# Optimization experiments

Hardware: AMD Instinct MI355X
Metric: run time of the kernel (lower is better)

## Reference

```python
import jax, jax.numpy as jnp
import numpy as np

N = 16384          # tokens
D = 2048           # model dim
SQRT_K = 64        # per-factor codebook size
K = SQRT_K * SQRT_K  # num_experts = 4096
TOP_K = 8
GATE_RANK = 16


def setup_inputs() -> dict:
    key = jax.random.key(0)
    k_x, k_w1, k_w2, k_wg, k_g = jax.random.split(key, 5)
    x = jax.random.normal(k_x, (N, D), dtype=jnp.float32)
    # nn.Linear(d, sqrt_K, bias=False) weights: [out, in]
    W1 = jax.random.normal(k_w1, (SQRT_K, D), dtype=jnp.float32) * (1.0 / np.sqrt(D))
    W2 = jax.random.normal(k_w2, (SQRT_K, D), dtype=jnp.float32) * (1.0 / np.sqrt(D))
    Wg = jax.random.normal(k_wg, (GATE_RANK, D), dtype=jnp.float32) * (1.0 / np.sqrt(D))
    # gate_keys: Parameter(randn(K, gate_rank) * 0.01)
    G = jax.random.normal(k_g, (K, GATE_RANK), dtype=jnp.float32) * 0.01
    return {"x": x, "W1": W1, "W2": W2, "Wg": Wg, "G": G}


def reference(x, W1, W2, Wg, G):
    # Stage 1: product-key selection scores
    s1 = x @ W1.T                                   # [N, sqrt_K]
    s2 = x @ W2.T                                   # [N, sqrt_K]
    select_scores = (s1[:, :, None] + s2[:, None, :]).reshape(x.shape[0], -1)  # [N, K]
    select_topk_vals, topk_idx = jax.lax.top_k(select_scores, TOP_K)           # [N, top_k]

    # Stage 2: low-rank gate calibration
    q_g = x @ Wg.T                                  # [N, r_g]
    gate_full = q_g @ G.T                           # [N, K]
    gate_topk = jnp.take_along_axis(gate_full, topk_idx, axis=-1)              # [N, top_k]

    combined = select_topk_vals + gate_topk
    topk_weights = jax.nn.softmax(combined, axis=-1)
    return topk_idx, topk_weights, select_scores
```

## Files before the change

### kernel.cpp

```cpp
#include <hip/hip_runtime.h>
#include <math.h>
#include <float.h>

#define NTOK  16384
#define DDIM  2048
#define TOPK  8
#define GR    16

#define MB    32
#define KB    64
#define WS_ST 148
#define XS_ST 34
#define S_ST  148
#define LDSF  (KB*WS_ST + KB*XS_ST)

__device__ __forceinline__ void insert8(float v[TOPK], int id[TOPK], float nv, int nk)
{
    bool beats_last = (nv > v[TOPK-1]) || (nv == v[TOPK-1] && nk < id[TOPK-1]);
    if (!beats_last) return;
    v[TOPK-1] = nv; id[TOPK-1] = nk;
    #pragma unroll
    for (int q = TOPK-1; q > 0; --q) {
        bool sw = (v[q] > v[q-1]) || (v[q] == v[q-1] && id[q] < id[q-1]);
        if (sw) {
            float tv = v[q]; v[q] = v[q-1]; v[q-1] = tv;
            int   ti = id[q]; id[q] = id[q-1]; id[q-1] = ti;
        }
    }
}

__global__ __launch_bounds__(256, 2) void pk_router(
    const float* __restrict__ x,  const float* __restrict__ W1,
    const float* __restrict__ W2, const float* __restrict__ Wg,
    const float* __restrict__ G,  float* __restrict__ out)
{
    __shared__ float lds[LDSF];
    const int t    = threadIdx.x;
    const int rb   = blockIdx.x * MB;
    const int rowg = t & 15;
    const int colg = t >> 4;

    float acc1[2][4];
    float acc2[2][4];
    float accg[2];
    #pragma unroll
    for (int r = 0; r < 2; ++r) {
        #pragma unroll
        for (int u = 0; u < 4; ++u) { acc1[r][u] = 0.f; acc2[r][u] = 0.f; }
        accg[r] = 0.f;
    }

    float* xs = lds + KB*WS_ST;

    for (int kb = 0; kb < DDIM; kb += KB) {
        #pragma unroll
        for (int i = 0; i < 2; ++i) {
            const int idx = t + 256*i;
            const int r   = idx >> 4;
            const int k4  = idx & 15;
            const float4 v = *(const float4*)(x + (size_t)(rb + r)*DDIM + kb + k4*4);
            xs[(k4*4+0)*XS_ST + r] = v.x;
            xs[(k4*4+1)*XS_ST + r] = v.y;
            xs[(k4*4+2)*XS_ST + r] = v.z;
            xs[(k4*4+3)*XS_ST + r] = v.w;
        }
        #pragma unroll
        for (int i = 0; i < 9; ++i) {
            const int idx = t + 256*i;
            const int c   = idx >> 4;
            const int k4  = idx & 15;
            const float* src = (c < 64)  ? (W1 + (size_t)c*DDIM)
                             : (c < 128) ? (W2 + (size_t)(c-64)*DDIM)
                                         : (Wg + (size_t)(c-128)*DDIM);
            const float4 v = *(const float4*)(src + kb + k4*4);
            lds[(k4*4+0)*WS_ST + c] = v.x;
            lds[(k4*4+1)*WS_ST + c] = v.y;
            lds[(k4*4+2)*WS_ST + c] = v.z;
            lds[(k4*4+3)*WS_ST + c] = v.w;
        }
        __syncthreads();

        #pragma unroll 8
        for (int kk = 0; kk < KB; ++kk) {
            const float2 a  = *(const float2*)(xs + kk*XS_ST + rowg*2);
            const float4 b1 = *(const float4*)(lds + kk*WS_ST + colg*4);
            const float4 b2 = *(const float4*)(lds + kk*WS_ST + 64 + colg*4);
            const float  bg = lds[kk*WS_ST + 128 + colg];
            acc1[0][0] += a.x*b1.x; acc1[0][1] += a.x*b1.y;
            acc1[0][2] += a.x*b1.z; acc1[0][3] += a.x*b1.w;
            acc1[1][0] += a.y*b1.x; acc1[1][1] += a.y*b1.y;
            acc1[1][2] += a.y*b1.z; acc1[1][3] += a.y*b1.w;
            acc2[0][0] += a.x*b2.x; acc2[0][1] += a.x*b2.y;
            acc2[0][2] += a.x*b2.z; acc2[0][3] += a.x*b2.w;
            acc2[1][0] += a.y*b2.x; acc2[1][1] += a.y*b2.y;
            acc2[1][2] += a.y*b2.z; acc2[1][3] += a.y*b2.w;
            accg[0] += a.x*bg;
            accg[1] += a.y*bg;
        }
        __syncthreads();
    }

    float* S = lds;
    #pragma unroll
    for (int rr = 0; rr < 2; ++rr) {
        const int r = rowg*2 + rr;
        #pragma unroll
        for (int u = 0; u < 4; ++u) {
            S[r*S_ST + colg*4 + u]      = acc1[rr][u];
            S[r*S_ST + 64 + colg*4 + u] = acc2[rr][u];
        }
        S[r*S_ST + 128 + colg] = accg[rr];
    }
    __syncthreads();

    const size_t scoreBase = (size_t)NTOK*2*TOPK + (size_t)rb*4096;
    const int i0 = t >> 4;
    const int j4 = (t & 15)*4;
    for (int r = 0; r < MB; ++r) {
        const float4 s2v = *(const float4*)(S + r*S_ST + 64 + j4);
        #pragma unroll
        for (int q = 0; q < 4; ++q) {
            const float s1v = S[r*S_ST + q*16 + i0];
            float4 o;
            o.x = s1v + s2v.x; o.y = s1v + s2v.y;
            o.z = s1v + s2v.z; o.w = s1v + s2v.w;
            *(float4*)(out + scoreBase + (size_t)r*4096 + (size_t)(q*1024 + t*4)) = o;
        }
    }

    if (t < MB) {
        const float* Srow = S + t*S_ST;
        float v1[TOPK], v2[TOPK]; int i1[TOPK], i2[TOPK];
        #pragma unroll
        for (int e = 0; e < TOPK; ++e) { v1[e] = -FLT_MAX; v2[e] = -FLT_MAX; i1[e] = 1<<30; i2[e] = 1<<30; }
        for (int i = 0; i < 64; ++i) insert8(v1, i1, Srow[i], i);
        for (int j = 0; j < 64; ++j) insert8(v2, i2, Srow[64 + j], j);

        float cv[TOPK]; int ck[TOPK];
        #pragma unroll
        for (int e = 0; e < TOPK; ++e) { cv[e] = -FLT_MAX; ck[e] = 1<<30; }
        #pragma unroll
        for (int a = 0; a < TOPK; ++a) {
            #pragma unroll
            for (int b = 0; b < TOPK; ++b)
                insert8(cv, ck, v1[a] + v2[b], i1[a]*64 + i2[b]);
        }

        float qg[GR];
        #pragma unroll
        for (int u = 0; u < GR; ++u) qg[u] = Srow[128 + u];

        float comb[TOPK];
        #pragma unroll
        for (int e = 0; e < TOPK; ++e) {
            const float* gp = G + (size_t)ck[e]*GR;
            float dot = 0.f;
            #pragma unroll
            for (int u = 0; u < GR; ++u) dot += qg[u] * gp[u];
            comb[e] = cv[e] + dot;
        }
        float m = comb[0];
        #pragma unroll
        for (int e = 1; e < TOPK; ++e) m = fmaxf(m, comb[e]);
        float w[TOPK]; float s = 0.f;
        #pragma unroll
        for (int e = 0; e < TOPK; ++e) { w[e] = expf(comb[e] - m); s += w[e]; }
        const float inv = 1.f / s;

        const size_t row = (size_t)rb + t;
        #pragma unroll
        for (int e = 0; e < TOPK; ++e) {
            out[row*TOPK + e] = (float)ck[e];
            out[(size_t)NTOK*TOPK + row*TOPK + e] = w[e]*inv;
        }
    }
}

extern "C" void kernel_launch(void* const* d_in, const int* in_sizes, int n_in,
                              void* d_out, int out_size, void* d_ws, size_t ws_size,
                              hipStream_t stream)
{
    const float* x  = (const float*)d_in[0];
    const float* W1 = (const float*)d_in[1];
    const float* W2 = (const float*)d_in[2];
    const float* Wg = (const float*)d_in[3];
    const float* G  = (const float*)d_in[4];
    float* out = (float*)d_out;

    pk_router<<<dim3(NTOK/MB), dim3(256), 0, stream>>>(x, W1, W2, Wg, G, out);
}
```

Baseline: 664.3 us.

## Restructure projection GEMM: wave-uniform weight loads, double-buffered x tiles, 64-row blocks

Each wave now owns 18 weight columns and reads them directly from global memory with wave-uniform addresses (scalar/broadcast loads), while each lane owns one token row of x. Only x is staged in LDS, double-buffered so the next tile is prefetched into registers during compute. The block grows to 512 threads and 64 rows, halving the grid. This removes LDS staging of the weight matrix and its transposed scatter stores, but makes weight reads depend on the cache and cuts per-thread reuse to one row of x.

```diff
diff --git a/kernel.cpp b/kernel.cpp
--- a/kernel.cpp
+++ b/kernel.cpp
@@ -6,13 +6,11 @@
 #define DDIM  2048
 #define TOPK  8
 #define GR    16
-
-#define MB    32
+#define ROWS  64
 #define KB    64
-#define WS_ST 148
-#define XS_ST 34
-#define S_ST  148
-#define LDSF  (KB*WS_ST + KB*XS_ST)
+#define XST   68
+#define SST   148
+#define CPW   18
 
 __device__ __forceinline__ void insert8(float v[TOPK], int id[TOPK], float nv, int nk)
 {
@@ -29,107 +27,100 @@
     }
 }
 
-__global__ __launch_bounds__(256, 2) void pk_router(
+__global__ __launch_bounds__(512, 2) void pk_router(
     const float* __restrict__ x,  const float* __restrict__ W1,
     const float* __restrict__ W2, const float* __restrict__ Wg,
     const float* __restrict__ G,  float* __restrict__ out)
 {
-    __shared__ float lds[LDSF];
+    __shared__ float lds[ROWS * SST];
+    float* xs0 = lds;
+    float* xs1 = lds + ROWS * XST;
+
     const int t    = threadIdx.x;
-    const int rb   = blockIdx.x * MB;
-    const int rowg = t & 15;
-    const int colg = t >> 4;
+    const int rb   = blockIdx.x * ROWS;
+    const int wid  = __builtin_amdgcn_readfirstlane(t >> 6);
+    const int lane = t & 63;
 
-    float acc1[2][4];
-    float acc2[2][4];
-    float accg[2];
+    const float* wp[CPW];
     #pragma unroll
-    for (int r = 0; r < 2; ++r) {
-        #pragma unroll
-        for (int u = 0; u < 4; ++u) { acc1[r][u] = 0.f; acc2[r][u] = 0.f; }
-        accg[r] = 0.f;
+    for (int c = 0; c < CPW; ++c) {
+        const int gc = wid * CPW + c;
+        wp[c] = (gc < 64)  ? (W1 + (size_t)gc * DDIM)
+              : (gc < 128) ? (W2 + (size_t)(gc - 64) * DDIM)
+                           : (Wg + (size_t)(gc - 128) * DDIM);
     }
 
-    float* xs = lds + KB*WS_ST;
+    float acc[CPW];
+    #pragma unroll
+    for (int c = 0; c < CPW; ++c) acc[c] = 0.f;
 
-    for (int kb = 0; kb < DDIM; kb += KB) {
-        #pragma unroll
-        for (int i = 0; i < 2; ++i) {
-            const int idx = t + 256*i;
-            const int r   = idx >> 4;
-            const int k4  = idx & 15;
-            const float4 v = *(const float4*)(x + (size_t)(rb + r)*DDIM + kb + k4*4);
-            xs[(k4*4+0)*XS_ST + r] = v.x;
-            xs[(k4*4+1)*XS_ST + r] = v.y;
-            xs[(k4*4+2)*XS_ST + r] = v.z;
-            xs[(k4*4+3)*XS_ST + r] = v.w;
-        }
-        #pragma unroll
-        for (int i = 0; i < 9; ++i) {
-            const int idx = t + 256*i;
-            const int c   = idx >> 4;
-            const int k4  = idx & 15;
-            const float* src = (c < 64)  ? (W1 + (size_t)c*DDIM)
-                             : (c < 128) ? (W2 + (size_t)(c-64)*DDIM)
-                                         : (Wg + (size_t)(c-128)*DDIM);
-            const float4 v = *(const float4*)(src + kb + k4*4);
-            lds[(k4*4+0)*WS_ST + c] = v.x;
-            lds[(k4*4+1)*WS_ST + c] = v.y;
-            lds[(k4*4+2)*WS_ST + c] = v.z;
-            lds[(k4*4+3)*WS_ST + c] = v.w;
-        }
-        __syncthreads();
+    const int sr0 = t >> 4;
+    const int sr1 = sr0 + 32;
+    const int sk0 = (t & 15) * 4;
+    const float* gx0 = x + (size_t)(rb + sr0) * DDIM + sk0;
+    const float* gx1 = x + (size_t)(rb + sr1) * DDIM + sk0;
 
-        #pragma unroll 8
-        for (int kk = 0; kk < KB; ++kk) {
-            const float2 a  = *(const float2*)(xs + kk*XS_ST + rowg*2);
-            const float4 b1 = *(const float4*)(lds + kk*WS_ST + colg*4);
-            const float4 b2 = *(const float4*)(lds + kk*WS_ST + 64 + colg*4);
-            const float  bg = lds[kk*WS_ST + 128 + colg];
-            acc1[0][0] += a.x*b1.x; acc1[0][1] += a.x*b1.y;
-            acc1[0][2] += a.x*b1.z; acc1[0][3] += a.x*b1.w;
-            acc1[1][0] += a.y*b1.x; acc1[1][1] += a.y*b1.y;
-            acc1[1][2] += a.y*b1.z; acc1[1][3] += a.y*b1.w;
-            acc2[0][0] += a.x*b2.x; acc2[0][1] += a.x*b2.y;
-            acc2[0][2] += a.x*b2.z; acc2[0][3] += a.x*b2.w;
-            acc2[1][0] += a.y*b2.x; acc2[1][1] += a.y*b2.y;
-            acc2[1][2] += a.y*b2.z; acc2[1][3] += a.y*b2.w;
-            accg[0] += a.x*bg;
-            accg[1] += a.y*bg;
-        }
-        __syncthreads();
-    }
-
-    float* S = lds;
-    #pragma unroll
-    for (int rr = 0; rr < 2; ++rr) {
-        const int r = rowg*2 + rr;
-        #pragma unroll
-        for (int u = 0; u < 4; ++u) {
-            S[r*S_ST + colg*4 + u]      = acc1[rr][u];
-            S[r*S_ST + 64 + colg*4 + u] = acc2[rr][u];
-        }
-        S[r*S_ST + 128 + colg] = accg[rr];
+    {
+        const float4 p0 = *(const float4*)(gx0);
+        const float4 p1 = *(const float4*)(gx1);
+        *(float4*)(xs0 + sr0 * XST + sk0) = p0;
+        *(float4*)(xs0 + sr1 * XST + sk0) = p1;
     }
     __syncthreads();
 
-    const size_t scoreBase = (size_t)NTOK*2*TOPK + (size_t)rb*4096;
-    const int i0 = t >> 4;
-    const int j4 = (t & 15)*4;
-    for (int r = 0; r < MB; ++r) {
-        const float4 s2v = *(const float4*)(S + r*S_ST + 64 + j4);
-        #pragma unroll
-        for (int q = 0; q < 4; ++q) {
-            const float s1v = S[r*S_ST + q*16 + i0];
-            float4 o;
-            o.x = s1v + s2v.x; o.y = s1v + s2v.y;
-            o.z = s1v + s2v.z; o.w = s1v + s2v.w;
-            *(float4*)(out + scoreBase + (size_t)r*4096 + (size_t)(q*1024 + t*4)) = o;
+    for (int kb = 0; kb < DDIM; kb += KB) {
+        float* xb = (kb & KB) ? xs1 : xs0;
+        float4 n0, n1;
+        const bool more = (kb + KB) < DDIM;
+        if (more) {
+            n0 = *(const float4*)(gx0 + kb + KB);
+            n1 = *(const float4*)(gx1 + kb + KB);
+        }
+        const float* xr = xb + lane * XST;
+        #pragma unroll 2
+        for (int kk = 0; kk < KB; kk += 4) {
+            const float4 a = *(const float4*)(xr + kk);
+            #pragma unroll
+            for (int c = 0; c < CPW; ++c) {
+                const float4 w = *(const float4*)(wp[c] + kb + kk);
+                acc[c] += a.x * w.x;
+                acc[c] += a.y * w.y;
+                acc[c] += a.z * w.z;
+                acc[c] += a.w * w.w;
+            }
+        }
+        __syncthreads();
+        if (more) {
+            float* xn = ((kb + KB) & KB) ? xs1 : xs0;
+            *(float4*)(xn + sr0 * XST + sk0) = n0;
+            *(float4*)(xn + sr1 * XST + sk0) = n1;
+            __syncthreads();
         }
     }
 
-    if (t < MB) {
-        const float* Srow = S + t*S_ST;
+    #pragma unroll
+    for (int c = 0; c < CPW; ++c)
+        lds[lane * SST + wid * CPW + c] = acc[c];
+    __syncthreads();
+
+    const size_t scoreBase = (size_t)NTOK * 2 * TOPK + (size_t)rb * 4096;
+    const int i0 = t >> 4;
+    const int j4 = (t & 15) * 4;
+    for (int r = 0; r < ROWS; ++r) {
+        const float* Sr = lds + r * SST;
+        const float4 s2v = *(const float4*)(Sr + 64 + j4);
+        const float s1a = Sr[i0];
+        const float s1b = Sr[i0 + 32];
+        float4 oa, ob;
+        oa.x = s1a + s2v.x; oa.y = s1a + s2v.y; oa.z = s1a + s2v.z; oa.w = s1a + s2v.w;
+        ob.x = s1b + s2v.x; ob.y = s1b + s2v.y; ob.z = s1b + s2v.z; ob.w = s1b + s2v.w;
+        float* od = out + scoreBase + (size_t)r * 4096;
+        *(float4*)(od + (size_t)(i0 * 64 + j4))        = oa;
+        *(float4*)(od + (size_t)((i0 + 32) * 64 + j4)) = ob;
+    }
+
+    if (t < ROWS) {
+        const float* Srow = lds + t * SST;
         float v1[TOPK], v2[TOPK]; int i1[TOPK], i2[TOPK];
         #pragma unroll
         for (int e = 0; e < TOPK; ++e) { v1[e] = -FLT_MAX; v2[e] = -FLT_MAX; i1[e] = 1<<30; i2[e] = 1<<30; }
@@ -153,7 +144,7 @@
         float comb[TOPK];
         #pragma unroll
         for (int e = 0; e < TOPK; ++e) {
-            const float* gp = G + (size_t)ck[e]*GR;
+            const float* gp = G + (size_t)ck[e] * GR;
             float dot = 0.f;
             #pragma unroll
             for (int u = 0; u < GR; ++u) dot += qg[u] * gp[u];
@@ -170,8 +161,8 @@
         const size_t row = (size_t)rb + t;
         #pragma unroll
         for (int e = 0; e < TOPK; ++e) {
-            out[row*TOPK + e] = (float)ck[e];
-            out[(size_t)NTOK*TOPK + row*TOPK + e] = w[e]*inv;
+            out[row * TOPK + e] = (float)ck[e];
+            out[(size_t)NTOK * TOPK + row * TOPK + e] = w[e] * inv;
         }
     }
 }
@@ -187,5 +178,5 @@
     const float* G  = (const float*)d_in[4];
     float* out = (float*)d_out;
 
-    pk_router<<<dim3(NTOK/MB), dim3(256), 0, stream>>>(x, W1, W2, Wg, G, out);
+    pk_router<<<dim3(NTOK / ROWS), dim3(512), 0, stream>>>(x, W1, W2, Wg, G, out);
 }
```

After: 1.033 ms. 1.56x slower.
